# Kernel tuning notes

Hardware: AMD Instinct MI355X
Metric: run time of the kernel (lower is better)

Reference implementation:

```python
import jax, jax.numpy as jnp
import numpy as np

B, C, L = 2, 512, 4096
HEADS, KV_HEADS, DIM_HEAD = 8, 2, 64
ROTARY_DIM = 32  # int(64 * 0.5), even
ROPE_THETA = 10000.0
SCALE = DIM_HEAD ** -0.5


def _rotate_half(x):
    # pairs (x0, x1) -> (-x1, x0), interleaved layout
    x = x.reshape(*x.shape[:-1], x.shape[-1] // 2, 2)
    x1, x2 = x[..., 0], x[..., 1]
    return jnp.stack([-x2, x1], axis=-1).reshape(*x.shape[:-2], x.shape[-2] * 2)


def _rope_sin_cos(seq_len, rotary_dim, theta, dtype):
    positions = jnp.arange(seq_len, dtype=dtype)
    half = rotary_dim // 2
    inv_freq = theta ** (-2.0 * jnp.arange(half, dtype=dtype) / rotary_dim)
    sinusoid = positions[:, None] * inv_freq[None, :]          # (L, half)
    sin = jnp.repeat(jnp.sin(sinusoid), 2, axis=-1)            # (L, rotary_dim) interleaved
    cos = jnp.repeat(jnp.cos(sinusoid), 2, axis=-1)
    return sin[None, None], cos[None, None]                    # (1,1,L,rotary_dim)


def setup_inputs() -> dict:
    key = jax.random.key(0)
    kx, kq, kkv, ko = jax.random.split(key, 4)
    s = 0.02
    return {
        "x": jax.random.normal(kx, (B, C, L), dtype=jnp.float32),
        "Wq": jax.random.normal(kq, (HEADS * DIM_HEAD, C), dtype=jnp.float32) * s,
        "Wkv": jax.random.normal(kkv, (2 * KV_HEADS * DIM_HEAD, C), dtype=jnp.float32) * s,
        "Wo": jax.random.normal(ko, (C, HEADS * DIM_HEAD), dtype=jnp.float32) * s,
    }


def reference(x, Wq, Wkv, Wo):
    b, c, l = x.shape
    x_t = jnp.swapaxes(x, 1, 2)                                 # (B, L, C)
    q = x_t @ Wq.T                                              # (B, L, H*dh)
    kv = x_t @ Wkv.T                                            # (B, L, KVH*2*dh)
    q = q.reshape(b, l, HEADS, DIM_HEAD).transpose(0, 2, 1, 3)  # (B, H, L, dh)
    kv = kv.reshape(b, l, KV_HEADS, 2 * DIM_HEAD).transpose(0, 2, 1, 3)
    k, v = jnp.split(kv, 2, axis=-1)                            # (B, KVH, L, dh) each

    sin, cos = _rope_sin_cos(l, ROTARY_DIM, ROPE_THETA, x.dtype)
    q_rot, q_pass = q[..., :ROTARY_DIM], q[..., ROTARY_DIM:]
    k_rot, k_pass = k[..., :ROTARY_DIM], k[..., ROTARY_DIM:]
    q_rot = q_rot * cos + _rotate_half(q_rot) * sin
    k_rot = k_rot * cos + _rotate_half(k_rot) * sin
    q = jnp.concatenate([q_rot, q_pass], axis=-1)
    k = jnp.concatenate([k_rot, k_pass], axis=-1)

    rep = HEADS // KV_HEADS
    k = jnp.repeat(k, rep, axis=1)                              # (B, H, L, dh)
    v = jnp.repeat(v, rep, axis=1)

    q = q * SCALE
    attn = jnp.einsum('bhid,bhjd->bhij', q, k)                  # (B, H, L, L)
    attn = jax.nn.softmax(attn, axis=-1)
    out = jnp.einsum('bhij,bhjd->bhid', attn, v)                # (B, H, L, dh)
    out = out.transpose(0, 2, 1, 3).reshape(b, l, HEADS * DIM_HEAD)
    out = out @ Wo.T                                            # (B, L, C)
    return jnp.swapaxes(out, 1, 2)                              # (B, C, L)
```

## Files before the change

kernel.cpp:

```cpp
#include <hip/hip_runtime.h>

using f16   = _Float16;
using f16x2 = __attribute__((ext_vector_type(2))) f16;
using f16x4 = __attribute__((ext_vector_type(4))) f16;
using f16x8 = __attribute__((ext_vector_type(8))) f16;
using f32x4 = __attribute__((ext_vector_type(4))) float;

#define L_ 4096
#define C_ 512

static __device__ __forceinline__ float fast_exp2(float x) {
#if __has_builtin(__builtin_amdgcn_exp2f)
  return __builtin_amdgcn_exp2f(x);
#else
  float r; asm("v_exp_f32 %0, %1" : "=v"(r) : "v"(x)); return r;
#endif
}

static __device__ __forceinline__ f16x2 pk2(float a, float b) {
  return __builtin_bit_cast(f16x2, __builtin_amdgcn_cvt_pkrtz(a, b));
}

#define WS_SC    0u
#define WS_WQKV  524288u
#define WS_WO    1310720u
#define WS_Q     1835008u
#define WS_K     10223616u
#define WS_VT    12320768u
#define WS_ATT   14417920u
#define WS_OP    22806528u
#define WS_LS2   56360960u
#define WS_END2  56885248u

__global__ __launch_bounds__(256) void prep_kernel(
    const float* __restrict__ Wq, const float* __restrict__ Wkv,
    const float* __restrict__ Wo,
    f16* __restrict__ wqkv, f16* __restrict__ wo16, float2* __restrict__ sc) {
  int t = blockIdx.x * 256 + threadIdx.x;
  if (t < 98304) {
    int idx = t * 4;
    float4 v = (idx < 262144) ? *(const float4*)(Wq + idx)
                              : *(const float4*)(Wkv + (idx - 262144));
    f16x4 o = {(f16)v.x, (f16)v.y, (f16)v.z, (f16)v.w};
    *(f16x4*)(wqkv + idx) = o;
  } else if (t < 163840) {
    int idx = (t - 98304) * 4;
    float4 v = *(const float4*)(Wo + idx);
    f16x4 o = {(f16)v.x, (f16)v.y, (f16)v.z, (f16)v.w};
    *(f16x4*)(wo16 + idx) = o;
  } else if (t < 229376) {
    int e = t - 163840;
    int l = e >> 4, p = e & 15;
    float invf = exp2f(-(float)p * (13.287712379549449f / 16.0f));
    float ang = (float)l * invf;
    sc[e] = make_float2(sinf(ang), cosf(ang));
  }
}

__global__ __launch_bounds__(256) void qkv_kernel(
    const float* __restrict__ x, const f16* __restrict__ wqkv,
    const float2* __restrict__ sc,
    f16* __restrict__ Qo, f16* __restrict__ Ko, f16* __restrict__ Vto) {
  int bid = blockIdx.x;
  int b   = bid / 384;
  int rem = bid % 384;
  int ot  = rem >> 7;
  int lt  = rem & 127;
  int wave = threadIdx.x >> 6, lane = threadIdx.x & 63;
  int lo = lane & 15, hi = lane >> 4;
  int obase = ot * 256 + wave * 64;
  int lbase = lt * 32;
  const float* xb = x + (size_t)b * C_ * L_;

  f32x4 acc[4][2] = {};
  for (int kc = 0; kc < 512; kc += 32) {
    f16x8 aw[4];
#pragma unroll
    for (int oc = 0; oc < 4; ++oc)
      aw[oc] = *(const f16x8*)(wqkv + (obase + oc * 16 + lo) * 512 + kc + hi * 8);
#pragma unroll
    for (int lc = 0; lc < 2; ++lc) {
      f16x8 bx;
#pragma unroll
      for (int i = 0; i < 8; ++i)
        bx[i] = (f16)xb[(size_t)(kc + hi * 8 + i) * L_ + lbase + lc * 16 + lo];
#pragma unroll
      for (int oc = 0; oc < 4; ++oc)
        acc[oc][lc] = __builtin_amdgcn_mfma_f32_16x16x32_f16(aw[oc], bx, acc[oc][lc], 0, 0, 0);
    }
  }

  bool is_q = obase < 512;
  int  og   = obase - 512;
  int  kvh  = is_q ? 0 : (og >> 7);
  bool is_v = (!is_q) && ((og & 127) == 64);
  int  h    = obase >> 6;
  const float QSCALE = 0.125f * 1.44269504088896340736f;

#pragma unroll
  for (int oc = 0; oc < 4; ++oc) {
#pragma unroll
    for (int lc = 0; lc < 2; ++lc) {
      f32x4 v = acc[oc][lc];
      int l = lbase + lc * 16 + lo;
      int d = oc * 16 + hi * 4;
      if (!is_v && oc < 2) {
        int p0 = d >> 1;
        float2 s0 = sc[l * 16 + p0];
        float2 s1 = sc[l * 16 + p0 + 1];
        float a0 = v[0], a1 = v[1], a2 = v[2], a3 = v[3];
        v[0] = a0 * s0.y - a1 * s0.x;
        v[1] = a1 * s0.y + a0 * s0.x;
        v[2] = a2 * s1.y - a3 * s1.x;
        v[3] = a3 * s1.y + a2 * s1.x;
      }
      if (is_q) {
        f16x4 st = {(f16)(v[0] * QSCALE), (f16)(v[1] * QSCALE),
                    (f16)(v[2] * QSCALE), (f16)(v[3] * QSCALE)};
        *(f16x4*)(Qo + (((size_t)b * 8 + h) * L_ + l) * 64 + d) = st;
      } else if (!is_v) {
        f16x4 st = {(f16)v[0], (f16)v[1], (f16)v[2], (f16)v[3]};
        *(f16x4*)(Ko + (((size_t)b * 2 + kvh) * L_ + l) * 64 + d) = st;
      } else {
#pragma unroll
        for (int i = 0; i < 4; ++i)
          Vto[(((size_t)b * 2 + kvh) * 64 + d + i) * L_ + l] = (f16)v[i];
      }
    }
  }
}

template <int SPLIT>
__global__ __launch_bounds__(512) void attn_kernel(
    const f16* __restrict__ Qi, const f16* __restrict__ Ki,
    const f16* __restrict__ Vti, f16* __restrict__ att,
    f16* __restrict__ opart, float* __restrict__ lsews) {
  __shared__ __align__(16) char smem[2][16384];
  int bid  = blockIdx.x;
  int half = (SPLIT > 1) ? (bid >> 8) : 0;
  int rem9 = bid & 255;
  int b   = rem9 >> 7;
  int rem = rem9 & 127;
  int h   = rem >> 4;
  int qt  = rem & 15;
  int tid  = threadIdx.x;
  int wave = tid >> 6, lane = tid & 63;
  int lo = lane & 15, hi = lane >> 4;
  int kvh = h >> 2;
  const f16*  Qp   = Qi + ((size_t)(b * 8 + h) * L_) * 64;
  const char* Ksrc = (const char*)(Ki  + ((size_t)(b * 2 + kvh)) * L_ * 64)
                     + (size_t)half * (L_ / SPLIT) * 128;
  const char* Vsrc = (const char*)(Vti + ((size_t)(b * 2 + kvh)) * 64 * L_)
                     + (size_t)half * (L_ / SPLIT) * 2;

  int lqb = qt * 256 + wave * 32;
  f16x8 qf[2][2];
#pragma unroll
  for (int qi = 0; qi < 2; ++qi)
#pragma unroll
    for (int hf = 0; hf < 2; ++hf)
      qf[qi][hf] = *(const f16x8*)(Qp + (size_t)(lqb + qi * 16 + lo) * 64 + hf * 32 + hi * 8);

  int c0 = tid;
  int r0 = c0 >> 3, m0 = c0 & 7;
  int cb0 = m0 << 4;
  int dstK0 = r0 * 128 + (cb0 ^ ((r0 & 7) << 4));
  int ca0 = (m0 >> 2) * 64 + ((2 * m0) & 3) * 16 + ((m0 >> 1) & 1) * 8;
  int dstV0a = r0 * 128 + (ca0 ^ ((r0 & 7) << 4));
  int dstV0b = r0 * 128 + ((ca0 + 16) ^ ((r0 & 7) << 4));

  f16x8 sK0, sV0;
#define STAGE_LOAD(t) do {                                            \
    sK0 = *(const f16x8*)(Ksrc + (size_t)(t) * 8192 + c0 * 16);       \
    sV0 = *(const f16x8*)(Vsrc + (size_t)r0 * 8192 + (t) * 128 + cb0);\
  } while (0)
#define STAGE_WRITE(base_) do {                                       \
    char* kb_ = (char*)(base_);                                       \
    *(f16x8*)(kb_ + dstK0) = sK0;                                     \
    *(f16x4*)(kb_ + 8192 + dstV0a) = __builtin_shufflevector(sV0, sV0, 0, 1, 2, 3); \
    *(f16x4*)(kb_ + 8192 + dstV0b) = __builtin_shufflevector(sV0, sV0, 4, 5, 6, 7); \
  } while (0)

  f32x4 oacc[4][2] = {};
  f32x4 lse[2] = {};
  const f16x8 ones8 = {(f16)1.f, (f16)1.f, (f16)1.f, (f16)1.f,
                       (f16)1.f, (f16)1.f, (f16)1.f, (f16)1.f};
  int swz = (lo & 7) << 4;

#define COMPUTE(buf_) do {                                                          \
    const char* kb = (const char*)(buf_);                                           \
    const char* vb = kb + 8192;                                                     \
    f32x4 s[4][2] = {};                                                             \
    __builtin_amdgcn_s_setprio(1);                                                  \
    _Pragma("unroll")                                                               \
    for (int j = 0; j < 4; ++j) {                                                   \
      f16x8 ka0 = *(const f16x8*)(kb + (j * 16 + lo) * 128 + ((hi * 16) ^ swz));    \
      f16x8 ka1 = *(const f16x8*)(kb + (j * 16 + lo) * 128 + ((64 + hi * 16) ^ swz));\
      _Pragma("unroll")                                                             \
      for (int qi = 0; qi < 2; ++qi) {                                              \
        s[j][qi] = __builtin_amdgcn_mfma_f32_16x16x32_f16(ka0, qf[qi][0], s[j][qi], 0, 0, 0); \
        s[j][qi] = __builtin_amdgcn_mfma_f32_16x16x32_f16(ka1, qf[qi][1], s[j][qi], 0, 0, 0); \
      }                                                                             \
    }                                                                               \
    __builtin_amdgcn_s_setprio(0);                                                  \
    f16x4 pf[4][2];                                                                 \
    _Pragma("unroll")                                                               \
    for (int qi = 0; qi < 2; ++qi)                                                  \
      _Pragma("unroll")                                                             \
      for (int j = 0; j < 4; ++j) {                                                 \
        f16x2 p01 = pk2(fast_exp2(s[j][qi][0]), fast_exp2(s[j][qi][1]));            \
        f16x2 p23 = pk2(fast_exp2(s[j][qi][2]), fast_exp2(s[j][qi][3]));            \
        pf[j][qi] = __builtin_shufflevector(p01, p23, 0, 1, 2, 3);                  \
      }                                                                             \
    f16x8 pc[2][2];                                                                 \
    _Pragma("unroll")                                                               \
    for (int qi = 0; qi < 2; ++qi) {                                                \
      pc[0][qi] = __builtin_shufflevector(pf[0][qi], pf[1][qi], 0, 1, 2, 3, 4, 5, 6, 7); \
      pc[1][qi] = __builtin_shufflevector(pf[2][qi], pf[3][qi], 0, 1, 2, 3, 4, 5, 6, 7); \
    }                                                                               \
    __builtin_amdgcn_s_setprio(1);                                                  \
    _Pragma("unroll")                                                               \
    for (int dc = 0; dc < 4; ++dc) {                                                \
      _Pragma("unroll")                                                             \
      for (int jp = 0; jp < 2; ++jp) {                                              \
        f16x8 vv = *(const f16x8*)(vb + (dc * 16 + lo) * 128 + ((jp * 64 + hi * 16) ^ swz)); \
        oacc[dc][0] = __builtin_amdgcn_mfma_f32_16x16x32_f16(vv, pc[jp][0], oacc[dc][0], 0, 0, 0); \
        oacc[dc][1] = __builtin_amdgcn_mfma_f32_16x16x32_f16(vv, pc[jp][1], oacc[dc][1], 0, 0, 0); \
      }                                                                             \
    }                                                                               \
    _Pragma("unroll")                                                               \
    for (int jp = 0; jp < 2; ++jp) {                                                \
      lse[0] = __builtin_amdgcn_mfma_f32_16x16x32_f16(ones8, pc[jp][0], lse[0], 0, 0, 0); \
      lse[1] = __builtin_amdgcn_mfma_f32_16x16x32_f16(ones8, pc[jp][1], lse[1], 0, 0, 0); \
    }                                                                               \
    __builtin_amdgcn_s_setprio(0);                                                  \
  } while (0)

  const int NT = 64 / SPLIT;
  STAGE_LOAD(0);
  STAGE_WRITE(smem[0]);
  __syncthreads();

  for (int t = 0; t < NT; t += 2) {
    STAGE_LOAD(t + 1);
    COMPUTE(smem[0]);
    STAGE_WRITE(smem[1]);
    __syncthreads();
    if (t + 2 < NT) STAGE_LOAD(t + 2);
    COMPUTE(smem[1]);
    if (t + 2 < NT) STAGE_WRITE(smem[0]);
    __syncthreads();
  }

#pragma unroll
  for (int qi = 0; qi < 2; ++qi) {
    int lq = lqb + qi * 16 + lo;
    if constexpr (SPLIT > 1) {
      size_t obase = (((size_t)(half * 2 + b) * 8 + h) * L_ + lq) * 64;
#pragma unroll
      for (int dc = 0; dc < 4; ++dc) {
        f16x4 st;
#pragma unroll
        for (int i = 0; i < 4; ++i) st[i] = (f16)oacc[dc][qi][i];
        *(f16x4*)(opart + obase + dc * 16 + hi * 4) = st;
      }
      if (hi == 0)
        lsews[((size_t)(half * 2 + b) * 8 + h) * L_ + lq] = lse[qi][0];
    } else {
      float inv = 1.f / lse[qi][0];
#pragma unroll
      for (int dc = 0; dc < 4; ++dc) {
        f16x4 st;
#pragma unroll
        for (int i = 0; i < 4; ++i) st[i] = (f16)(oacc[dc][qi][i] * inv);
        *(f16x4*)(att + ((size_t)b * L_ + lq) * 512 + h * 64 + dc * 16 + hi * 4) = st;
      }
    }
  }
#undef STAGE_LOAD
#undef STAGE_WRITE
#undef COMPUTE
}

template <int SPLIT>
__global__ __launch_bounds__(256) void combine_kernel(
    const f16* __restrict__ opart, const float* __restrict__ lsews,
    f16* __restrict__ att) {
  int t = blockIdx.x * 256 + threadIdx.x;
  int d4 = t & 15;
  int lq = (t >> 4) & 4095;
  int h  = (t >> 16) & 7;
  int b  = t >> 19;
  const size_t HS  = (size_t)2 * 8 * 4096 * 64;
  const size_t LSS = (size_t)2 * 8 * 4096;
  size_t base  = (((size_t)b * 8 + h) * 4096 + lq) * 64 + d4 * 4;
  size_t lbase = ((size_t)b * 8 + h) * 4096 + lq;
  float o[4] = {};
  float ls = 0.f;
#pragma unroll
  for (int s = 0; s < SPLIT; ++s) {
    f16x4 op = *(const f16x4*)(opart + s * HS + base);
#pragma unroll
    for (int i = 0; i < 4; ++i) o[i] += (float)op[i];
    ls += lsews[s * LSS + lbase];
  }
  float inv = 1.f / ls;
  f16x4 st;
#pragma unroll
  for (int i = 0; i < 4; ++i) st[i] = (f16)(o[i] * inv);
  *(f16x4*)(att + ((size_t)b * 4096 + lq) * 512 + h * 64 + d4 * 4) = st;
}

__global__ __launch_bounds__(256) void oproj_kernel(
    const f16* __restrict__ att, const f16* __restrict__ wo16,
    float* __restrict__ out) {
  int bid = blockIdx.x;
  int b   = bid / 256;
  int rem = bid % 256;
  int ct  = rem >> 7;
  int lt  = rem & 127;
  int wave = threadIdx.x >> 6, lane = threadIdx.x & 63;
  int lo = lane & 15, hi = lane >> 4;
  int cobase = ct * 256 + wave * 64;
  int lbase  = lt * 32;
  const f16* ab = att + (size_t)b * L_ * 512;

  f32x4 acc[4][2] = {};
  for (int kc = 0; kc < 512; kc += 32) {
    f16x8 aw[4];
#pragma unroll
    for (int cc = 0; cc < 4; ++cc)
      aw[cc] = *(const f16x8*)(wo16 + (cobase + cc * 16 + lo) * 512 + kc + hi * 8);
#pragma unroll
    for (int lc = 0; lc < 2; ++lc) {
      f16x8 bx = *(const f16x8*)(ab + (size_t)(lbase + lc * 16 + lo) * 512 + kc + hi * 8);
#pragma unroll
      for (int cc = 0; cc < 4; ++cc)
        acc[cc][lc] = __builtin_amdgcn_mfma_f32_16x16x32_f16(aw[cc], bx, acc[cc][lc], 0, 0, 0);
    }
  }
  float* ob = out + (size_t)b * C_ * L_;
#pragma unroll
  for (int cc = 0; cc < 4; ++cc)
#pragma unroll
    for (int lc = 0; lc < 2; ++lc) {
      int l = lbase + lc * 16 + lo;
#pragma unroll
      for (int i = 0; i < 4; ++i) {
        int co = cobase + cc * 16 + hi * 4 + i;
        ob[(size_t)co * L_ + l] = acc[cc][lc][i];
      }
    }
}

extern "C" void kernel_launch(void* const* d_in, const int* in_sizes, int n_in,
                              void* d_out, int out_size, void* d_ws, size_t ws_size,
                              hipStream_t stream) {
  const float* x   = (const float*)d_in[0];
  const float* Wq  = (const float*)d_in[1];
  const float* Wkv = (const float*)d_in[2];
  const float* Wo  = (const float*)d_in[3];
  char* ws = (char*)d_ws;
  float2* sc  = (float2*)(ws + WS_SC);
  f16* wqkv   = (f16*)(ws + WS_WQKV);
  f16* wo16   = (f16*)(ws + WS_WO);
  f16* Qb     = (f16*)(ws + WS_Q);
  f16* Kb     = (f16*)(ws + WS_K);
  f16* Vtb    = (f16*)(ws + WS_VT);
  f16* attb   = (f16*)(ws + WS_ATT);
  f16* opb    = (f16*)(ws + WS_OP);
  float* lsb  = (float*)(ws + WS_LS2);

  prep_kernel<<<1024, 256, 0, stream>>>(Wq, Wkv, Wo, wqkv, wo16, sc);
  qkv_kernel<<<768, 256, 0, stream>>>(x, wqkv, sc, Qb, Kb, Vtb);
  if (ws_size >= (size_t)WS_END2) {
    attn_kernel<2><<<512, 512, 0, stream>>>(Qb, Kb, Vtb, attb, opb, lsb);
    combine_kernel<2><<<4096, 256, 0, stream>>>(opb, lsb, attb);
  } else {
    attn_kernel<1><<<256, 512, 0, stream>>>(Qb, Kb, Vtb, attb, opb, lsb);
  }
  oproj_kernel<<<512, 256, 0, stream>>>(attb, wo16, (float*)d_out);
}
```

Before: 150.0 us.

## Double query rows per wave and interleave QK/PV per key half-tile

Each wave now handles 64 query rows instead of 32, so every block covers 512 queries and the grid is halved. Each K/V tile loaded into shared memory is reused across twice as many queries, cutting global and LDS traffic per FLOP. The compute loop is also restructured to score, exponentiate and accumulate each 32-key half-tile before the next, which keeps register pressure bounded despite the doubled accumulators. The trade-off is higher VGPR use and only 256 blocks on a GPU with many CUs, so occupancy and tail balance may suffer.

Measured after the change: 144.5 us. 3.6% less time.

```diff
diff --git a/kernel.cpp b/kernel.cpp
--- a/kernel.cpp
+++ b/kernel.cpp
@@ -137,12 +137,12 @@
     f16* __restrict__ opart, float* __restrict__ lsews) {
   __shared__ __align__(16) char smem[2][16384];
   int bid  = blockIdx.x;
-  int half = (SPLIT > 1) ? (bid >> 8) : 0;
-  int rem9 = bid & 255;
-  int b   = rem9 >> 7;
-  int rem = rem9 & 127;
-  int h   = rem >> 4;
-  int qt  = rem & 15;
+  int half = (SPLIT > 1) ? (bid >> 7) : 0;
+  int rem7 = bid & 127;
+  int b   = rem7 >> 6;
+  int rr  = rem7 & 63;
+  int h   = rr >> 3;
+  int qt  = rr & 7;
   int tid  = threadIdx.x;
   int wave = tid >> 6, lane = tid & 63;
   int lo = lane & 15, hi = lane >> 4;
@@ -153,10 +153,10 @@
   const char* Vsrc = (const char*)(Vti + ((size_t)(b * 2 + kvh)) * 64 * L_)
                      + (size_t)half * (L_ / SPLIT) * 2;
 
-  int lqb = qt * 256 + wave * 32;
-  f16x8 qf[2][2];
-#pragma unroll
-  for (int qi = 0; qi < 2; ++qi)
+  int lqb = qt * 512 + wave * 64;
+  f16x8 qf[4][2];
+#pragma unroll
+  for (int qi = 0; qi < 4; ++qi)
 #pragma unroll
     for (int hf = 0; hf < 2; ++hf)
       qf[qi][hf] = *(const f16x8*)(Qp + (size_t)(lqb + qi * 16 + lo) * 64 + hf * 32 + hi * 8);
@@ -181,8 +181,8 @@
     *(f16x4*)(kb_ + 8192 + dstV0b) = __builtin_shufflevector(sV0, sV0, 4, 5, 6, 7); \
   } while (0)
 
-  f32x4 oacc[4][2] = {};
-  f32x4 lse[2] = {};
+  f32x4 oacc[4][4] = {};
+  f32x4 lse[4] = {};
   const f16x8 ones8 = {(f16)1.f, (f16)1.f, (f16)1.f, (f16)1.f,
                        (f16)1.f, (f16)1.f, (f16)1.f, (f16)1.f};
   int swz = (lo & 7) << 4;
@@ -190,50 +190,46 @@
 #define COMPUTE(buf_) do {                                                          \
     const char* kb = (const char*)(buf_);                                           \
     const char* vb = kb + 8192;                                                     \
-    f32x4 s[4][2] = {};                                                             \
-    __builtin_amdgcn_s_setprio(1);                                                  \
-    _Pragma("unroll")                                                               \
-    for (int j = 0; j < 4; ++j) {                                                   \
-      f16x8 ka0 = *(const f16x8*)(kb + (j * 16 + lo) * 128 + ((hi * 16) ^ swz));    \
-      f16x8 ka1 = *(const f16x8*)(kb + (j * 16 + lo) * 128 + ((64 + hi * 16) ^ swz));\
-      _Pragma("unroll")                                                             \
-      for (int qi = 0; qi < 2; ++qi) {                                              \
-        s[j][qi] = __builtin_amdgcn_mfma_f32_16x16x32_f16(ka0, qf[qi][0], s[j][qi], 0, 0, 0); \
-        s[j][qi] = __builtin_amdgcn_mfma_f32_16x16x32_f16(ka1, qf[qi][1], s[j][qi], 0, 0, 0); \
-      }                                                                             \
-    }                                                                               \
-    __builtin_amdgcn_s_setprio(0);                                                  \
-    f16x4 pf[4][2];                                                                 \
-    _Pragma("unroll")                                                               \
-    for (int qi = 0; qi < 2; ++qi)                                                  \
-      _Pragma("unroll")                                                             \
-      for (int j = 0; j < 4; ++j) {                                                 \
-        f16x2 p01 = pk2(fast_exp2(s[j][qi][0]), fast_exp2(s[j][qi][1]));            \
-        f16x2 p23 = pk2(fast_exp2(s[j][qi][2]), fast_exp2(s[j][qi][3]));            \
-        pf[j][qi] = __builtin_shufflevector(p01, p23, 0, 1, 2, 3);                  \
-      }                                                                             \
-    f16x8 pc[2][2];                                                                 \
-    _Pragma("unroll")                                                               \
-    for (int qi = 0; qi < 2; ++qi) {                                                \
-      pc[0][qi] = __builtin_shufflevector(pf[0][qi], pf[1][qi], 0, 1, 2, 3, 4, 5, 6, 7); \
-      pc[1][qi] = __builtin_shufflevector(pf[2][qi], pf[3][qi], 0, 1, 2, 3, 4, 5, 6, 7); \
-    }                                                                               \
-    __builtin_amdgcn_s_setprio(1);                                                  \
-    _Pragma("unroll")                                                               \
-    for (int dc = 0; dc < 4; ++dc) {                                                \
-      _Pragma("unroll")                                                             \
-      for (int jp = 0; jp < 2; ++jp) {                                              \
-        f16x8 vv = *(const f16x8*)(vb + (dc * 16 + lo) * 128 + ((jp * 64 + hi * 16) ^ swz)); \
-        oacc[dc][0] = __builtin_amdgcn_mfma_f32_16x16x32_f16(vv, pc[jp][0], oacc[dc][0], 0, 0, 0); \
-        oacc[dc][1] = __builtin_amdgcn_mfma_f32_16x16x32_f16(vv, pc[jp][1], oacc[dc][1], 0, 0, 0); \
-      }                                                                             \
-    }                                                                               \
     _Pragma("unroll")                                                               \
     for (int jp = 0; jp < 2; ++jp) {                                                \
-      lse[0] = __builtin_amdgcn_mfma_f32_16x16x32_f16(ones8, pc[jp][0], lse[0], 0, 0, 0); \
-      lse[1] = __builtin_amdgcn_mfma_f32_16x16x32_f16(ones8, pc[jp][1], lse[1], 0, 0, 0); \
+      f32x4 s[2][4] = {};                                                           \
+      __builtin_amdgcn_s_setprio(1);                                                \
+      _Pragma("unroll")                                                             \
+      for (int jj = 0; jj < 2; ++jj) {                                              \
+        int j = jp * 2 + jj;                                                        \
+        f16x8 ka0 = *(const f16x8*)(kb + (j * 16 + lo) * 128 + ((hi * 16) ^ swz));  \
+        f16x8 ka1 = *(const f16x8*)(kb + (j * 16 + lo) * 128 + ((64 + hi * 16) ^ swz)); \
+        _Pragma("unroll")                                                           \
+        for (int qi = 0; qi < 4; ++qi) {                                            \
+          s[jj][qi] = __builtin_amdgcn_mfma_f32_16x16x32_f16(ka0, qf[qi][0], s[jj][qi], 0, 0, 0); \
+          s[jj][qi] = __builtin_amdgcn_mfma_f32_16x16x32_f16(ka1, qf[qi][1], s[jj][qi], 0, 0, 0); \
+        }                                                                           \
+      }                                                                             \
+      __builtin_amdgcn_s_setprio(0);                                                \
+      f16x8 pc[4];                                                                  \
+      _Pragma("unroll")                                                             \
+      for (int qi = 0; qi < 4; ++qi) {                                              \
+        f16x2 a0 = pk2(fast_exp2(s[0][qi][0]), fast_exp2(s[0][qi][1]));             \
+        f16x2 a1 = pk2(fast_exp2(s[0][qi][2]), fast_exp2(s[0][qi][3]));             \
+        f16x2 b0 = pk2(fast_exp2(s[1][qi][0]), fast_exp2(s[1][qi][1]));             \
+        f16x2 b1 = pk2(fast_exp2(s[1][qi][2]), fast_exp2(s[1][qi][3]));             \
+        f16x4 l4 = __builtin_shufflevector(a0, a1, 0, 1, 2, 3);                     \
+        f16x4 h4 = __builtin_shufflevector(b0, b1, 0, 1, 2, 3);                     \
+        pc[qi] = __builtin_shufflevector(l4, h4, 0, 1, 2, 3, 4, 5, 6, 7);           \
+      }                                                                             \
+      __builtin_amdgcn_s_setprio(1);                                                \
+      _Pragma("unroll")                                                             \
+      for (int dc = 0; dc < 4; ++dc) {                                              \
+        f16x8 vv = *(const f16x8*)(vb + (dc * 16 + lo) * 128 + ((jp * 64 + hi * 16) ^ swz)); \
+        _Pragma("unroll")                                                           \
+        for (int qi = 0; qi < 4; ++qi)                                              \
+          oacc[dc][qi] = __builtin_amdgcn_mfma_f32_16x16x32_f16(vv, pc[qi], oacc[dc][qi], 0, 0, 0); \
+      }                                                                             \
+      _Pragma("unroll")                                                             \
+      for (int qi = 0; qi < 4; ++qi)                                                \
+        lse[qi] = __builtin_amdgcn_mfma_f32_16x16x32_f16(ones8, pc[qi], lse[qi], 0, 0, 0); \
+      __builtin_amdgcn_s_setprio(0);                                                \
     }                                                                               \
-    __builtin_amdgcn_s_setprio(0);                                                  \
   } while (0)
 
   const int NT = 64 / SPLIT;
@@ -253,7 +249,7 @@
   }
 
 #pragma unroll
-  for (int qi = 0; qi < 2; ++qi) {
+  for (int qi = 0; qi < 4; ++qi) {
     int lq = lqb + qi * 16 + lo;
     if constexpr (SPLIT > 1) {
       size_t obase = (((size_t)(half * 2 + b) * 8 + h) * L_ + lq) * 64;
@@ -374,10 +370,10 @@
   prep_kernel<<<1024, 256, 0, stream>>>(Wq, Wkv, Wo, wqkv, wo16, sc);
   qkv_kernel<<<768, 256, 0, stream>>>(x, wqkv, sc, Qb, Kb, Vtb);
   if (ws_size >= (size_t)WS_END2) {
-    attn_kernel<2><<<512, 512, 0, stream>>>(Qb, Kb, Vtb, attb, opb, lsb);
+    attn_kernel<2><<<256, 512, 0, stream>>>(Qb, Kb, Vtb, attb, opb, lsb);
     combine_kernel<2><<<4096, 256, 0, stream>>>(opb, lsb, attb);
   } else {
-    attn_kernel<1><<<256, 512, 0, stream>>>(Qb, Kb, Vtb, attb, opb, lsb);
+    attn_kernel<1><<<128, 512, 0, stream>>>(Qb, Kb, Vtb, attb, opb, lsb);
   }
   oproj_kernel<<<512, 256, 0, stream>>>(attb, wo16, (float*)d_out);
 }
```
